# Kernel tuning notes

Measured on AMD Instinct MI355X. Metric: run time of the kernel, lower is better.

The kernel has to match this reference:

```python
import jax, jax.numpy as jnp
import numpy as np

B, S, E, H, D = 4, 2048, 1024, 8, 256  # batch, seq, embed_dim, heads, hidden_units


def setup_inputs() -> dict:
    key = jax.random.key(0)
    ks = jax.random.split(key, 9)
    scale = 0.02
    return {
        "inputA": jax.random.normal(ks[0], (B, S, E), dtype=jnp.float32),
        "WQ": jax.random.normal(ks[1], (H, E, D), dtype=jnp.float32) * scale,
        "bQ": jnp.zeros((H, D), dtype=jnp.float32),
        "WK": jax.random.normal(ks[2], (H, E, D), dtype=jnp.float32) * scale,
        "bK": jnp.zeros((H, D), dtype=jnp.float32),
        "WV": jax.random.normal(ks[3], (H, E, D), dtype=jnp.float32) * scale,
        "bV": jnp.zeros((H, D), dtype=jnp.float32),
        "WZ": jax.random.normal(ks[4], (H * D, E), dtype=jnp.float32) * scale,
        "bZ": jnp.zeros((E,), dtype=jnp.float32),
    }


def reference(inputA, WQ, bQ, WK, bK, WV, bV, WZ, bZ):
    # Per-head Linear -> ReLU (dropout=0 -> identity); heads stacked on axis h.
    Q = jax.nn.relu(jnp.einsum('bse,hed->bhsd', inputA, WQ) + bQ[None, :, None, :])
    K = jax.nn.relu(jnp.einsum('bse,hed->bhsd', inputA, WK) + bK[None, :, None, :])
    V = jax.nn.relu(jnp.einsum('bse,hed->bhsd', inputA, WV) + bV[None, :, None, :])
    # scores[b,h,s,t] ; torch bmm output was [B, S, T] per head
    scores = jnp.einsum('bhsd,bhtd->bhst', Q, K) / jnp.sqrt(jnp.float32(E))
    # double softmax: torch dim=1 (query axis s) then dim=2 (key axis t)
    A = jax.nn.softmax(scores, axis=2)
    A = jax.nn.softmax(A, axis=3)
    Z = jnp.einsum('bhst,bhtd->bhsd', A, V)
    # concat heads along feature dim (head order matches torch cat)
    Zall = Z.transpose(0, 2, 1, 3).reshape(B, S, H * D)
    return Zall @ WZ + bZ
```

## Files before the change

kernel.cpp:

```cpp
#include <hip/hip_runtime.h>

typedef __attribute__((ext_vector_type(8))) short short8;
typedef __attribute__((ext_vector_type(4))) float f32x4;

constexpr int B_ = 4, S_ = 2048, E_ = 1024, H_ = 8, D_ = 256;
constexpr int HD_ = H_ * D_;
constexpr int BS_ = B_ * S_;
constexpr int BH_ = B_ * H_;
constexpr float INV_SQRT_E = 0.03125f;

__device__ __forceinline__ unsigned short f2bf(float f) {
    union { float f; unsigned u; } x; x.f = f;
    unsigned r = (x.u + 0x7fffu + ((x.u >> 16) & 1u)) >> 16;
    return (unsigned short)r;
}

__device__ __forceinline__ void gl_lds16(const void* g, void* lds) {
    __builtin_amdgcn_global_load_lds((const __attribute__((address_space(1))) void*)g,
                                     (__attribute__((address_space(3))) void*)lds, 16, 0, 0);
}

__global__ __launch_bounds__(256) void cast_k(const float* __restrict__ src,
                                              unsigned short* __restrict__ dst, int n4) {
    int i = blockIdx.x * 256 + threadIdx.x;
    if (i >= n4) return;
    float4 v = reinterpret_cast<const float4*>(src)[i];
    ushort4 o;
    o.x = f2bf(v.x); o.y = f2bf(v.y); o.z = f2bf(v.z); o.w = f2bf(v.w);
    reinterpret_cast<ushort4*>(dst)[i] = o;
}

__global__ __launch_bounds__(256) void tcast_k(const float* __restrict__ src,
                                               unsigned short* __restrict__ dst, int R, int C) {
    __shared__ float tile[32][33];
    int b = blockIdx.z;
    const float* s = src + (size_t)b * R * C;
    unsigned short* d = dst + (size_t)b * R * C;
    int c0 = blockIdx.x * 32, r0 = blockIdx.y * 32;
    int tx = threadIdx.x, ty = threadIdx.y;
#pragma unroll
    for (int i = 0; i < 4; ++i)
        tile[ty + i * 8][tx] = s[(size_t)(r0 + ty + i * 8) * C + c0 + tx];
    __syncthreads();
#pragma unroll
    for (int i = 0; i < 4; ++i)
        d[(size_t)(c0 + ty + i * 8) * R + r0 + tx] = f2bf(tile[tx][ty + i * 8]);
}

__global__ __launch_bounds__(256) void tbf_k(const unsigned short* __restrict__ src,
                                             unsigned short* __restrict__ dst) {
    __shared__ unsigned short tile[32][33];
    int bh = blockIdx.z;
    int d0 = blockIdx.x * 32, s0 = blockIdx.y * 32;
    int tx = threadIdx.x, ty = threadIdx.y;
#pragma unroll
    for (int i = 0; i < 4; ++i)
        tile[ty + i * 8][tx] = src[((size_t)bh * S_ + s0 + ty + i * 8) * D_ + d0 + tx];
    __syncthreads();
#pragma unroll
    for (int i = 0; i < 4; ++i)
        dst[((size_t)bh * D_ + d0 + ty + i * 8) * S_ + s0 + tx] = tile[tx][ty + i * 8];
}

__global__ __launch_bounds__(256) void gemm_qkv_k(const unsigned short* __restrict__ A,
                                                  const unsigned short* __restrict__ Bt,
                                                  const float* __restrict__ bias,
                                                  unsigned short* __restrict__ out) {
    __shared__ __align__(16) unsigned short As[128 * 32];
    __shared__ __align__(16) unsigned short Bs[128 * 32];
    const int tid = threadIdx.x;
    const int wave = tid >> 6, lane = tid & 63;
    const int quad = lane >> 4, l15 = lane & 15;
    const int wm = wave >> 1, wn = wave & 1;
    const int m0 = blockIdx.y * 128, n0 = blockIdx.x * 128;
    const int c1 = tid, c2 = tid + 256;
    const int r1 = c1 >> 2, kc1 = (c1 & 3) * 8;
    const int r2 = c2 >> 2, kc2 = (c2 & 3) * 8;
    char* aB1 = (char*)As + wave * 1024; char* aB2 = aB1 + 4096;
    char* bB1 = (char*)Bs + wave * 1024; char* bB2 = bB1 + 4096;
    const unsigned short* a1 = A + (size_t)(m0 + r1) * E_ + kc1;
    const unsigned short* a2 = A + (size_t)(m0 + r2) * E_ + kc2;
    const unsigned short* b1 = Bt + (size_t)(n0 + r1) * E_ + kc1;
    const unsigned short* b2 = Bt + (size_t)(n0 + r2) * E_ + kc2;
    f32x4 acc[4][4] = {};
    for (int k0 = 0; k0 < E_; k0 += 32) {
        __syncthreads();
        gl_lds16(a1 + k0, aB1);
        gl_lds16(a2 + k0, aB2);
        gl_lds16(b1 + k0, bB1);
        gl_lds16(b2 + k0, bB2);
        __syncthreads();
        short8 af[4], bf[4];
        const short* Ass = (const short*)As;
        const short* Bss = (const short*)Bs;
#pragma unroll
        for (int f = 0; f < 4; ++f) {
            af[f] = *(const short8*)&Ass[(wm * 64 + f * 16 + l15) * 32 + quad * 8];
            bf[f] = *(const short8*)&Bss[(wn * 64 + f * 16 + l15) * 32 + quad * 8];
        }
#pragma unroll
        for (int fm = 0; fm < 4; ++fm)
#pragma unroll
            for (int fn = 0; fn < 4; ++fn)
                acc[fm][fn] = __builtin_amdgcn_mfma_f32_16x16x32_bf16(af[fm], bf[fn], acc[fm][fn], 0, 0, 0);
    }
#pragma unroll
    for (int fm = 0; fm < 4; ++fm) {
        int mbase = m0 + wm * 64 + fm * 16 + quad * 4;
#pragma unroll
        for (int fn = 0; fn < 4; ++fn) {
            int n = n0 + wn * 64 + fn * 16 + l15;
            int h = n >> 8, d = n & 255;
            float bv = bias[n];
#pragma unroll
            for (int r = 0; r < 4; ++r) {
                int m = mbase + r;
                int b = m >> 11, s = m & 2047;
                float v = fmaxf(acc[fm][fn][r] + bv, 0.0f);
                out[((size_t)(b * H_ + h) * S_ + s) * D_ + d] = f2bf(v);
            }
        }
    }
}

__global__ __launch_bounds__(256) void gemm_out_k(const unsigned short* __restrict__ A,
                                                  const unsigned short* __restrict__ Bt,
                                                  const float* __restrict__ bias,
                                                  float* __restrict__ out) {
    __shared__ __align__(16) unsigned short As[128 * 32];
    __shared__ __align__(16) unsigned short Bs[128 * 32];
    const int tid = threadIdx.x;
    const int wave = tid >> 6, lane = tid & 63;
    const int quad = lane >> 4, l15 = lane & 15;
    const int wm = wave >> 1, wn = wave & 1;
    const int m0 = blockIdx.y * 128, n0 = blockIdx.x * 128;
    const int c1 = tid, c2 = tid + 256;
    const int r1 = c1 >> 2, kc1 = (c1 & 3) * 8;
    const int r2 = c2 >> 2, kc2 = (c2 & 3) * 8;
    char* aB1 = (char*)As + wave * 1024; char* aB2 = aB1 + 4096;
    char* bB1 = (char*)Bs + wave * 1024; char* bB2 = bB1 + 4096;
    const unsigned short* a1 = A + (size_t)(m0 + r1) * HD_ + kc1;
    const unsigned short* a2 = A + (size_t)(m0 + r2) * HD_ + kc2;
    const unsigned short* b1 = Bt + (size_t)(n0 + r1) * HD_ + kc1;
    const unsigned short* b2 = Bt + (size_t)(n0 + r2) * HD_ + kc2;
    f32x4 acc[4][4] = {};
    for (int k0 = 0; k0 < HD_; k0 += 32) {
        __syncthreads();
        gl_lds16(a1 + k0, aB1);
        gl_lds16(a2 + k0, aB2);
        gl_lds16(b1 + k0, bB1);
        gl_lds16(b2 + k0, bB2);
        __syncthreads();
        short8 af[4], bf[4];
        const short* Ass = (const short*)As;
        const short* Bss = (const short*)Bs;
#pragma unroll
        for (int f = 0; f < 4; ++f) {
            af[f] = *(const short8*)&Ass[(wm * 64 + f * 16 + l15) * 32 + quad * 8];
            bf[f] = *(const short8*)&Bss[(wn * 64 + f * 16 + l15) * 32 + quad * 8];
        }
#pragma unroll
        for (int fm = 0; fm < 4; ++fm)
#pragma unroll
            for (int fn = 0; fn < 4; ++fn)
                acc[fm][fn] = __builtin_amdgcn_mfma_f32_16x16x32_bf16(af[fm], bf[fn], acc[fm][fn], 0, 0, 0);
    }
#pragma unroll
    for (int fm = 0; fm < 4; ++fm) {
        int mbase = m0 + wm * 64 + fm * 16 + quad * 4;
#pragma unroll
        for (int fn = 0; fn < 4; ++fn) {
            int n = n0 + wn * 64 + fn * 16 + l15;
            float bv = bias[n];
#pragma unroll
            for (int r = 0; r < 4; ++r)
                out[(size_t)(mbase + r) * E_ + n] = acc[fm][fn][r] + bv;
        }
    }
}

__global__ __launch_bounds__(256) void colsum_k(const unsigned short* __restrict__ Q,
                                                const unsigned short* __restrict__ K,
                                                float* __restrict__ invLcol) {
    __shared__ __align__(16) unsigned short Ks[8 * 64 * 32];
    __shared__ float part[4][64];
    const int tid = threadIdx.x;
    const int wave = tid >> 6, lane = tid & 63;
    const int quad = lane >> 4, l15 = lane & 15;
    const int bh = blockIdx.y;
    const int t0 = blockIdx.x * 64;
    const unsigned short* Qh = Q + (size_t)bh * S_ * D_;
    const unsigned short* Kh = K + (size_t)bh * S_ * D_;
    const int sr = tid >> 2, scol = (tid & 3) * 8;
#pragma unroll
    for (int kc = 0; kc < 8; ++kc)
        gl_lds16(Kh + (size_t)(t0 + sr) * D_ + kc * 32 + scol,
                 (char*)Ks + kc * 4096 + wave * 1024);
    __syncthreads();
    float rl[4][4] = {};
    for (int s0 = 0; s0 < S_; s0 += 128) {
        f32x4 acc[4][2] = {};
#pragma unroll
        for (int kc = 0; kc < 8; ++kc) {
            short8 af[4];
#pragma unroll
            for (int fm = 0; fm < 4; ++fm)
                af[fm] = *(const short8*)&Ks[kc * 2048 + (fm * 16 + l15) * 32 + quad * 8];
            short8 qb0 = *(const short8*)&Qh[(size_t)(s0 + wave * 32 + l15) * D_ + kc * 32 + quad * 8];
            short8 qb1 = *(const short8*)&Qh[(size_t)(s0 + wave * 32 + 16 + l15) * D_ + kc * 32 + quad * 8];
#pragma unroll
            for (int fm = 0; fm < 4; ++fm) {
                acc[fm][0] = __builtin_amdgcn_mfma_f32_16x16x32_bf16(af[fm], qb0, acc[fm][0], 0, 0, 0);
                acc[fm][1] = __builtin_amdgcn_mfma_f32_16x16x32_bf16(af[fm], qb1, acc[fm][1], 0, 0, 0);
            }
        }
#pragma unroll
        for (int fm = 0; fm < 4; ++fm)
#pragma unroll
            for (int r = 0; r < 4; ++r)
                rl[fm][r] += __expf(acc[fm][0][r] * INV_SQRT_E) +
                             __expf(acc[fm][1][r] * INV_SQRT_E);
    }
#pragma unroll
    for (int fm = 0; fm < 4; ++fm)
#pragma unroll
        for (int r = 0; r < 4; ++r) {
            float v = rl[fm][r];
            v += __shfl_xor(v, 1); v += __shfl_xor(v, 2);
            v += __shfl_xor(v, 4); v += __shfl_xor(v, 8);
            if (l15 == 0) part[wave][fm * 16 + quad * 4 + r] = v;
        }
    __syncthreads();
    if (tid < 64) {
        float s = part[0][tid] + part[1][tid] + part[2][tid] + part[3][tid];
        invLcol[(size_t)bh * S_ + t0 + tid] = 1.0f / s;
    }
}

__global__ __launch_bounds__(256, 3) void flash6_k(const unsigned short* __restrict__ Q,
                                                   const unsigned short* __restrict__ K,
                                                   const unsigned short* __restrict__ Vt,
                                                   const float* __restrict__ invLcol,
                                                   unsigned short* __restrict__ Zall) {
    __shared__ __align__(16) unsigned short Qs[8 * 64 * 32];
    __shared__ __align__(16) unsigned short Ps[2 * 64 * 40];
    __shared__ float rsum[64];
    const int tid = threadIdx.x;
    const int wave = tid >> 6, lane = tid & 63;
    const int quad = lane >> 4, l15 = lane & 15;
    const int bh = blockIdx.y;
    const int bb = bh >> 3, hh = bh & 7;
    const int s0 = blockIdx.x * 64;
    const unsigned short* Qh = Q + (size_t)bh * S_ * D_;
    const unsigned short* Kh = K + (size_t)bh * S_ * D_;
    const unsigned short* Vh = Vt + (size_t)bh * D_ * S_;
    const float* Lc = invLcol + (size_t)bh * S_;
    const int sr = tid >> 2, scol = (tid & 3) * 8;
#pragma unroll
    for (int kc = 0; kc < 8; ++kc)
        gl_lds16(Qh + (size_t)(s0 + sr) * D_ + kc * 32 + scol,
                 (char*)Qs + kc * 4096 + wave * 1024);
    if (tid < 64) rsum[tid] = 0.f;
    f32x4 zacc[4][4] = {};
    float rsacc[4][4] = {};
    __syncthreads();
    for (int t0 = 0; t0 < S_; t0 += 64) {
        f32x4 acc[4] = {};
        float Li = Lc[t0 + wave * 16 + l15];
#pragma unroll
        for (int kc = 0; kc < 8; ++kc) {
            short8 kb = *(const short8*)&Kh[(size_t)(t0 + wave * 16 + l15) * D_ + kc * 32 + quad * 8];
#pragma unroll
            for (int fm = 0; fm < 4; ++fm) {
                short8 af = *(const short8*)&Qs[kc * 2048 + (fm * 16 + l15) * 32 + quad * 8];
                acc[fm] = __builtin_amdgcn_mfma_f32_16x16x32_bf16(af, kb, acc[fm], 0, 0, 0);
            }
        }
#pragma unroll
        for (int fm = 0; fm < 4; ++fm)
#pragma unroll
            for (int r = 0; r < 4; ++r) {
                float e = __expf(__expf(acc[fm][r] * INV_SQRT_E) * Li);
                rsacc[fm][r] += e;
                int row = fm * 16 + quad * 4 + r;
                Ps[(wave >> 1) * 2560 + row * 40 + (wave & 1) * 16 + l15] = f2bf(e);
            }
        __syncthreads();
#pragma unroll
        for (int kk = 0; kk < 2; ++kk) {
            short8 pa[4], vb[4];
#pragma unroll
            for (int fm = 0; fm < 4; ++fm)
                pa[fm] = *(const short8*)&Ps[kk * 2560 + (fm * 16 + l15) * 40 + quad * 8];
#pragma unroll
            for (int fn = 0; fn < 4; ++fn)
                vb[fn] = *(const short8*)&Vh[(size_t)(wave * 64 + fn * 16 + l15) * S_ + t0 + kk * 32 + quad * 8];
#pragma unroll
            for (int fm = 0; fm < 4; ++fm)
#pragma unroll
                for (int fn = 0; fn < 4; ++fn)
                    zacc[fm][fn] = __builtin_amdgcn_mfma_f32_16x16x32_bf16(pa[fm], vb[fn], zacc[fm][fn], 0, 0, 0);
        }
        __syncthreads();
    }
#pragma unroll
    for (int fm = 0; fm < 4; ++fm)
#pragma unroll
        for (int r = 0; r < 4; ++r) {
            float v = rsacc[fm][r];
            v += __shfl_xor(v, 1); v += __shfl_xor(v, 2);
            v += __shfl_xor(v, 4); v += __shfl_xor(v, 8);
            if (l15 == 0) atomicAdd(&rsum[fm * 16 + quad * 4 + r], v);
        }
    __syncthreads();
#pragma unroll
    for (int fm = 0; fm < 4; ++fm)
#pragma unroll
        for (int r = 0; r < 4; ++r) {
            int row = fm * 16 + quad * 4 + r;
            float inv = 1.0f / rsum[row];
#pragma unroll
            for (int fn = 0; fn < 4; ++fn)
                Zall[(size_t)(bb * S_ + s0 + row) * HD_ + hh * D_ + wave * 64 + fn * 16 + l15] =
                    f2bf(zacc[fm][fn][r] * inv);
        }
}

extern "C" void kernel_launch(void* const* d_in, const int* in_sizes, int n_in,
                              void* d_out, int out_size, void* d_ws, size_t ws_size,
                              hipStream_t stream) {
    const float* Ain = (const float*)d_in[0];
    const float* WQ = (const float*)d_in[1];
    const float* bQ = (const float*)d_in[2];
    const float* WK = (const float*)d_in[3];
    const float* bK = (const float*)d_in[4];
    const float* WV = (const float*)d_in[5];
    const float* bV = (const float*)d_in[6];
    const float* WZ = (const float*)d_in[7];
    const float* bZ = (const float*)d_in[8];
    float* out = (float*)d_out;

    char* ws = (char*)d_ws;
    size_t off = 0;
    auto alloc = [&](size_t bytes) {
        char* p = ws + off;
        off += (bytes + 255) & ~(size_t)255;
        return p;
    };
    unsigned short* Abf = (unsigned short*)alloc((size_t)BS_ * E_ * 2);
    unsigned short* Wqt = (unsigned short*)alloc((size_t)H_ * D_ * E_ * 2);
    unsigned short* Wkt = (unsigned short*)alloc((size_t)H_ * D_ * E_ * 2);
    unsigned short* Wvt = (unsigned short*)alloc((size_t)H_ * D_ * E_ * 2);
    unsigned short* Wzt = (unsigned short*)alloc((size_t)E_ * HD_ * 2);
    unsigned short* Qb = (unsigned short*)alloc((size_t)BH_ * S_ * D_ * 2);
    unsigned short* Kb = (unsigned short*)alloc((size_t)BH_ * S_ * D_ * 2);
    unsigned short* Vb = (unsigned short*)alloc((size_t)BH_ * S_ * D_ * 2);
    unsigned short* Vtb = (unsigned short*)alloc((size_t)BH_ * S_ * D_ * 2);
    unsigned short* Zb = (unsigned short*)alloc((size_t)BS_ * HD_ * 2);
    float* Lc = (float*)alloc((size_t)BH_ * S_ * 4);

    dim3 tb(32, 8);
    cast_k<<<(BS_ * E_ / 4 + 255) / 256, 256, 0, stream>>>(Ain, Abf, BS_ * E_ / 4);
    tcast_k<<<dim3(D_ / 32, E_ / 32, H_), tb, 0, stream>>>(WQ, Wqt, E_, D_);
    tcast_k<<<dim3(D_ / 32, E_ / 32, H_), tb, 0, stream>>>(WK, Wkt, E_, D_);
    tcast_k<<<dim3(D_ / 32, E_ / 32, H_), tb, 0, stream>>>(WV, Wvt, E_, D_);
    tcast_k<<<dim3(E_ / 32, HD_ / 32, 1), tb, 0, stream>>>(WZ, Wzt, HD_, E_);

    gemm_qkv_k<<<dim3(HD_ / 128, BS_ / 128), 256, 0, stream>>>(Abf, Wqt, bQ, Qb);
    gemm_qkv_k<<<dim3(HD_ / 128, BS_ / 128), 256, 0, stream>>>(Abf, Wkt, bK, Kb);
    gemm_qkv_k<<<dim3(HD_ / 128, BS_ / 128), 256, 0, stream>>>(Abf, Wvt, bV, Vb);

    tbf_k<<<dim3(D_ / 32, S_ / 32, BH_), tb, 0, stream>>>(Vb, Vtb);

    colsum_k<<<dim3(S_ / 64, BH_), 256, 0, stream>>>(Qb, Kb, Lc);
    flash6_k<<<dim3(S_ / 64, BH_), 256, 0, stream>>>(Qb, Kb, Vtb, Lc, Zb);

    gemm_out_k<<<dim3(E_ / 128, BS_ / 128), 256, 0, stream>>>(Zb, Wzt, bZ, out);
}
```

Measured before the change: 770.5 us.

## Hold Q/K tiles in registers and double-buffer P to drop a barrier

Both attention kernels now keep their 64-row operand tile (K in colsum, Q in the flash kernel) in registers as 32 short8 fragments instead of staging it through LDS. The flash kernel also double-buffers the P tile in shared memory, which removes the trailing barrier per key block, and it prefetches K and V fragments ahead of the MFMAs. The aim is less LDS traffic and fewer synchronisations. The cost is much higher VGPR pressure, with occupancy hints lowered to 2 blocks per SIMD.

Result: no change. 777.5 us (+0.9%).

```diff
diff --git a/kernel.cpp b/kernel.cpp
--- a/kernel.cpp
+++ b/kernel.cpp
@@ -179,10 +179,9 @@
     }
 }
 
-__global__ __launch_bounds__(256) void colsum_k(const unsigned short* __restrict__ Q,
-                                                const unsigned short* __restrict__ K,
-                                                float* __restrict__ invLcol) {
-    __shared__ __align__(16) unsigned short Ks[8 * 64 * 32];
+__global__ __launch_bounds__(256, 2) void colsum_k(const unsigned short* __restrict__ Q,
+                                                   const unsigned short* __restrict__ K,
+                                                   float* __restrict__ invLcol) {
     __shared__ float part[4][64];
     const int tid = threadIdx.x;
     const int wave = tid >> 6, lane = tid & 63;
@@ -191,35 +190,30 @@
     const int t0 = blockIdx.x * 64;
     const unsigned short* Qh = Q + (size_t)bh * S_ * D_;
     const unsigned short* Kh = K + (size_t)bh * S_ * D_;
-    const int sr = tid >> 2, scol = (tid & 3) * 8;
+    short8 kf[32];
 #pragma unroll
     for (int kc = 0; kc < 8; ++kc)
-        gl_lds16(Kh + (size_t)(t0 + sr) * D_ + kc * 32 + scol,
-                 (char*)Ks + kc * 4096 + wave * 1024);
-    __syncthreads();
+#pragma unroll
+        for (int fm = 0; fm < 4; ++fm)
+            kf[kc * 4 + fm] = *(const short8*)&Kh[(size_t)(t0 + fm * 16 + l15) * D_ + kc * 32 + quad * 8];
     float rl[4][4] = {};
-    for (int s0 = 0; s0 < S_; s0 += 128) {
-        f32x4 acc[4][2] = {};
-#pragma unroll
-        for (int kc = 0; kc < 8; ++kc) {
-            short8 af[4];
+    const unsigned short* Qw = Qh + (size_t)(wave * 16 + l15) * D_ + quad * 8;
+    for (int s0 = 0; s0 < S_; s0 += 64) {
+        short8 qf[8];
+#pragma unroll
+        for (int kc = 0; kc < 8; ++kc)
+            qf[kc] = *(const short8*)&Qw[(size_t)s0 * D_ + kc * 32];
+        f32x4 acc[4] = {};
+#pragma unroll
+        for (int kc = 0; kc < 8; ++kc)
 #pragma unroll
             for (int fm = 0; fm < 4; ++fm)
-                af[fm] = *(const short8*)&Ks[kc * 2048 + (fm * 16 + l15) * 32 + quad * 8];
-            short8 qb0 = *(const short8*)&Qh[(size_t)(s0 + wave * 32 + l15) * D_ + kc * 32 + quad * 8];
-            short8 qb1 = *(const short8*)&Qh[(size_t)(s0 + wave * 32 + 16 + l15) * D_ + kc * 32 + quad * 8];
-#pragma unroll
-            for (int fm = 0; fm < 4; ++fm) {
-                acc[fm][0] = __builtin_amdgcn_mfma_f32_16x16x32_bf16(af[fm], qb0, acc[fm][0], 0, 0, 0);
-                acc[fm][1] = __builtin_amdgcn_mfma_f32_16x16x32_bf16(af[fm], qb1, acc[fm][1], 0, 0, 0);
-            }
-        }
+                acc[fm] = __builtin_amdgcn_mfma_f32_16x16x32_bf16(kf[kc * 4 + fm], qf[kc], acc[fm], 0, 0, 0);
 #pragma unroll
         for (int fm = 0; fm < 4; ++fm)
 #pragma unroll
             for (int r = 0; r < 4; ++r)
-                rl[fm][r] += __expf(acc[fm][0][r] * INV_SQRT_E) +
-                             __expf(acc[fm][1][r] * INV_SQRT_E);
+                rl[fm][r] += __expf(acc[fm][r] * INV_SQRT_E);
     }
 #pragma unroll
     for (int fm = 0; fm < 4; ++fm)
@@ -237,13 +231,12 @@
     }
 }
 
-__global__ __launch_bounds__(256, 3) void flash6_k(const unsigned short* __restrict__ Q,
+__global__ __launch_bounds__(256, 2) void flash7_k(const unsigned short* __restrict__ Q,
                                                    const unsigned short* __restrict__ K,
                                                    const unsigned short* __restrict__ Vt,
                                                    const float* __restrict__ invLcol,
                                                    unsigned short* __restrict__ Zall) {
-    __shared__ __align__(16) unsigned short Qs[8 * 64 * 32];
-    __shared__ __align__(16) unsigned short Ps[2 * 64 * 40];
+    __shared__ __align__(16) unsigned short Ps[2 * 2 * 64 * 40];
     __shared__ float rsum[64];
     const int tid = threadIdx.x;
     const int wave = tid >> 6, lane = tid & 63;
@@ -255,26 +248,33 @@
     const unsigned short* Kh = K + (size_t)bh * S_ * D_;
     const unsigned short* Vh = Vt + (size_t)bh * D_ * S_;
     const float* Lc = invLcol + (size_t)bh * S_;
-    const int sr = tid >> 2, scol = (tid & 3) * 8;
+
+    short8 q[32];
 #pragma unroll
     for (int kc = 0; kc < 8; ++kc)
-        gl_lds16(Qh + (size_t)(s0 + sr) * D_ + kc * 32 + scol,
-                 (char*)Qs + kc * 4096 + wave * 1024);
+#pragma unroll
+        for (int fm = 0; fm < 4; ++fm)
+            q[kc * 4 + fm] = *(const short8*)&Qh[(size_t)(s0 + fm * 16 + l15) * D_ + kc * 32 + quad * 8];
+
     if (tid < 64) rsum[tid] = 0.f;
     f32x4 zacc[4][4] = {};
     float rsacc[4][4] = {};
-    __syncthreads();
+
     for (int t0 = 0; t0 < S_; t0 += 64) {
+        const int pb = ((t0 >> 6) & 1) * 5120;
+        float Li = Lc[t0 + wave * 16 + l15];
+        const unsigned short* Kt = Kh + (size_t)(t0 + wave * 16 + l15) * D_ + quad * 8;
         f32x4 acc[4] = {};
-        float Li = Lc[t0 + wave * 16 + l15];
+        short8 kb[4];
+#pragma unroll
+        for (int kc = 0; kc < 4; ++kc) kb[kc] = *(const short8*)&Kt[kc * 32];
 #pragma unroll
         for (int kc = 0; kc < 8; ++kc) {
-            short8 kb = *(const short8*)&Kh[(size_t)(t0 + wave * 16 + l15) * D_ + kc * 32 + quad * 8];
-#pragma unroll
-            for (int fm = 0; fm < 4; ++fm) {
-                short8 af = *(const short8*)&Qs[kc * 2048 + (fm * 16 + l15) * 32 + quad * 8];
-                acc[fm] = __builtin_amdgcn_mfma_f32_16x16x32_bf16(af, kb, acc[fm], 0, 0, 0);
-            }
+            short8 kbu = kb[kc & 3];
+            if (kc < 4) kb[kc & 3] = *(const short8*)&Kt[(kc + 4) * 32];
+#pragma unroll
+            for (int fm = 0; fm < 4; ++fm)
+                acc[fm] = __builtin_amdgcn_mfma_f32_16x16x32_bf16(q[kc * 4 + fm], kbu, acc[fm], 0, 0, 0);
         }
 #pragma unroll
         for (int fm = 0; fm < 4; ++fm)
@@ -283,25 +283,34 @@
                 float e = __expf(__expf(acc[fm][r] * INV_SQRT_E) * Li);
                 rsacc[fm][r] += e;
                 int row = fm * 16 + quad * 4 + r;
-                Ps[(wave >> 1) * 2560 + row * 40 + (wave & 1) * 16 + l15] = f2bf(e);
+                Ps[pb + (wave >> 1) * 2560 + row * 40 + (wave & 1) * 16 + l15] = f2bf(e);
             }
-        __syncthreads();
-#pragma unroll
-        for (int kk = 0; kk < 2; ++kk) {
-            short8 pa[4], vb[4];
-#pragma unroll
-            for (int fm = 0; fm < 4; ++fm)
-                pa[fm] = *(const short8*)&Ps[kk * 2560 + (fm * 16 + l15) * 40 + quad * 8];
-#pragma unroll
-            for (int fn = 0; fn < 4; ++fn)
-                vb[fn] = *(const short8*)&Vh[(size_t)(wave * 64 + fn * 16 + l15) * S_ + t0 + kk * 32 + quad * 8];
-#pragma unroll
-            for (int fm = 0; fm < 4; ++fm)
-#pragma unroll
-                for (int fn = 0; fn < 4; ++fn)
-                    zacc[fm][fn] = __builtin_amdgcn_mfma_f32_16x16x32_bf16(pa[fm], vb[fn], zacc[fm][fn], 0, 0, 0);
-        }
-        __syncthreads();
+        const unsigned short* Vw = Vh + (size_t)(wave * 64 + l15) * S_ + t0 + quad * 8;
+        short8 vb[4];
+#pragma unroll
+        for (int fn = 0; fn < 4; ++fn)
+            vb[fn] = *(const short8*)&Vw[(size_t)(fn * 16) * S_];
+        __syncthreads();
+        short8 pa[4];
+#pragma unroll
+        for (int fm = 0; fm < 4; ++fm)
+            pa[fm] = *(const short8*)&Ps[pb + (fm * 16 + l15) * 40 + quad * 8];
+#pragma unroll
+        for (int fm = 0; fm < 4; ++fm)
+#pragma unroll
+            for (int fn = 0; fn < 4; ++fn)
+                zacc[fm][fn] = __builtin_amdgcn_mfma_f32_16x16x32_bf16(pa[fm], vb[fn], zacc[fm][fn], 0, 0, 0);
+#pragma unroll
+        for (int fn = 0; fn < 4; ++fn)
+            vb[fn] = *(const short8*)&Vw[(size_t)(fn * 16) * S_ + 32];
+#pragma unroll
+        for (int fm = 0; fm < 4; ++fm)
+            pa[fm] = *(const short8*)&Ps[pb + 2560 + (fm * 16 + l15) * 40 + quad * 8];
+#pragma unroll
+        for (int fm = 0; fm < 4; ++fm)
+#pragma unroll
+            for (int fn = 0; fn < 4; ++fn)
+                zacc[fm][fn] = __builtin_amdgcn_mfma_f32_16x16x32_bf16(pa[fm], vb[fn], zacc[fm][fn], 0, 0, 0);
     }
 #pragma unroll
     for (int fm = 0; fm < 4; ++fm)
@@ -373,7 +382,7 @@
     tbf_k<<<dim3(D_ / 32, S_ / 32, BH_), tb, 0, stream>>>(Vb, Vtb);
 
     colsum_k<<<dim3(S_ / 64, BH_), 256, 0, stream>>>(Qb, Kb, Lc);
-    flash6_k<<<dim3(S_ / 64, BH_), 256, 0, stream>>>(Qb, Kb, Vtb, Lc, Zb);
+    flash7_k<<<dim3(S_ / 64, BH_), 256, 0, stream>>>(Qb, Kb, Vtb, Lc, Zb);
 
     gemm_out_k<<<dim3(E_ / 128, BS_ / 128), 256, 0, stream>>>(Zb, Wzt, bZ, out);
 }
```
